# Optimization experiments

Hardware: AMD Instinct MI355X
Metric: run time of the kernel (lower is better)

The kernel has to match this reference:

```python
import jax, jax.numpy as jnp
import numpy as np

N_NODES = 50000
N_EDGES = 1600000
IN_DIM = 128
HID = [128, 128]
OUT_DIM = 64
N_USERS = 10000


def setup_inputs() -> dict:
    key = jax.random.key(0)
    ks = jax.random.split(key, 12)
    features = jax.random.normal(ks[0], (N_NODES, IN_DIM), jnp.float32)
    src = jax.random.randint(ks[1], (N_EDGES,), 0, N_NODES)
    dst = jax.random.randint(ks[2], (N_EDGES,), 0, N_NODES)
    users = jax.random.randint(ks[3], (N_USERS,), 0, N_NODES)
    s = 0.05
    W0 = jax.random.normal(ks[4], (IN_DIM, HID[0]), jnp.float32) * s
    b0 = jnp.zeros((HID[0],), jnp.float32)
    W1 = jax.random.normal(ks[5], (HID[0], HID[1]), jnp.float32) * s
    b1 = jnp.zeros((HID[1],), jnp.float32)
    Ws1 = jax.random.normal(ks[6], (HID[1], 64), jnp.float32) * s
    bs1 = jnp.zeros((64,), jnp.float32)
    Ws2 = jax.random.normal(ks[7], (64, OUT_DIM), jnp.float32) * s
    bs2 = jnp.zeros((OUT_DIM,), jnp.float32)
    return {"features": features, "W0": W0, "b0": b0, "W1": W1, "b1": b1,
            "Ws1": Ws1, "bs1": bs1, "Ws2": Ws2, "bs2": bs2,
            "src": src, "dst": dst, "users": users}


def _gcn_layer(h, src, dst, cs, cd, W, b):
    # DGL GraphConv, norm='both': relu(D_in^-1/2 A D_out^-1/2 (h W) + b)
    h = h @ W                                   # [N, d_out]
    m = (h * cs)[src]                           # [E, d_out] gathered messages
    agg = jax.ops.segment_sum(m, dst, num_segments=N_NODES)
    return jax.nn.relu(agg * cd + b)


def reference(features, W0, b0, W1, b1, Ws1, bs1, Ws2, bs2, src, dst, users):
    ones = jnp.ones(src.shape[0], jnp.float32)
    deg_out = jax.ops.segment_sum(ones, src, num_segments=N_NODES)
    deg_in = jax.ops.segment_sum(ones, dst, num_segments=N_NODES)
    cs = jnp.maximum(deg_out, 1.0)[:, None] ** -0.5  # source-side norm
    cd = jnp.maximum(deg_in, 1.0)[:, None] ** -0.5   # dest-side norm
    h = _gcn_layer(features, src, dst, cs, cd, W0, b0)
    # dropout between layers: identity in eval mode
    h = _gcn_layer(h, src, dst, cs, cd, W1, b1)
    user_h = h[users]                            # [U, HID[-1]]
    R = jnp.tanh(user_h @ Ws1 + bs1) @ Ws2 + bs2  # SR head
    return (R, h)
```

## Files before the change

kernel.cpp:

```cpp
#include <hip/hip_runtime.h>
#include <hip/hip_bf16.h>
#include <hip/hip_fp16.h>

#define NN 50000
#define NE 1600000
#define DIM 128
#define NU 10000
#define NB 256
#define SLICE_W 12500
#define NE4 (NE / 4)
#define CHUNK4 ((NE4 + NB - 1) / NB)
#define NSC 49

__global__ __launch_bounds__(512) void k_hist(const int4* __restrict__ src4,
                                              const int4* __restrict__ dst4,
                                              unsigned int* __restrict__ histD,
                                              unsigned int* __restrict__ histS) {
    __shared__ unsigned int lh[SLICE_W];
    for (int i = threadIdx.x; i < SLICE_W; i += 512) lh[i] = 0u;
    __syncthreads();
    int b = blockIdx.x & (NB - 1);
    const int4* idx4 = (blockIdx.x < NB) ? dst4 : src4;
    unsigned int* out = ((blockIdx.x < NB) ? histD : histS) + (size_t)b * SLICE_W;
    int beg = b * CHUNK4, end = min(beg + CHUNK4, NE4);
    for (int i = beg + threadIdx.x; i < end; i += 512) {
        int4 v = idx4[i];
        atomicAdd(&lh[v.x >> 2], 1u << ((v.x & 3) * 8));
        atomicAdd(&lh[v.y >> 2], 1u << ((v.y & 3) * 8));
        atomicAdd(&lh[v.z >> 2], 1u << ((v.z & 3) * 8));
        atomicAdd(&lh[v.w >> 2], 1u << ((v.w & 3) * 8));
    }
    __syncthreads();
    for (int i = threadIdx.x; i < SLICE_W; i += 512) out[i] = lh[i];
}

__global__ __launch_bounds__(256) void k_reduce_norms(const unsigned int* __restrict__ histD,
                                                      const unsigned int* __restrict__ histS,
                                                      int* __restrict__ din,
                                                      float* __restrict__ cs, float* __restrict__ cd,
                                                      int* __restrict__ partials) {
    __shared__ int red[256];
    int wi = blockIdx.x * blockDim.x + threadIdx.x;
    unsigned int d0 = 0, d1 = 0, d2 = 0, d3 = 0, s0 = 0, s1 = 0, s2 = 0, s3 = 0;
    if (wi < SLICE_W) {
        for (int b = 0; b < NB; ++b) {
            unsigned int wd = histD[(size_t)b * SLICE_W + wi];
            unsigned int ws = histS[(size_t)b * SLICE_W + wi];
            d0 += wd & 0xFFu; d1 += (wd >> 8) & 0xFFu; d2 += (wd >> 16) & 0xFFu; d3 += wd >> 24;
            s0 += ws & 0xFFu; s1 += (ws >> 8) & 0xFFu; s2 += (ws >> 16) & 0xFFu; s3 += ws >> 24;
        }
        int n = wi * 4;
        *(int4*)&din[n] = make_int4(d0, d1, d2, d3);
        float4 vcd, vcs;
        vcd.x = rsqrtf(fmaxf((float)d0, 1.f)); vcd.y = rsqrtf(fmaxf((float)d1, 1.f));
        vcd.z = rsqrtf(fmaxf((float)d2, 1.f)); vcd.w = rsqrtf(fmaxf((float)d3, 1.f));
        vcs.x = rsqrtf(fmaxf((float)s0, 1.f)); vcs.y = rsqrtf(fmaxf((float)s1, 1.f));
        vcs.z = rsqrtf(fmaxf((float)s2, 1.f)); vcs.w = rsqrtf(fmaxf((float)s3, 1.f));
        *(float4*)&cd[n] = vcd;
        *(float4*)&cs[n] = vcs;
    }
    red[threadIdx.x] = (int)(d0 + d1 + d2 + d3);
    __syncthreads();
    for (int off = 128; off > 0; off >>= 1) {
        if (threadIdx.x < off) red[threadIdx.x] += red[threadIdx.x + off];
        __syncthreads();
    }
    if (threadIdx.x == 0) partials[blockIdx.x] = red[0];
}

__global__ __launch_bounds__(64) void k_scan2(const int* __restrict__ partials,
                                              int* __restrict__ bases) {
    int lane = threadIdx.x;
    int v = (lane < NSC) ? partials[lane] : 0;
    int s = v;
    for (int off = 1; off < 64; off <<= 1) {
        int n = __shfl_up(s, off);
        if (lane >= off) s += n;
    }
    if (lane < NSC) bases[lane] = s - v;
}

__global__ __launch_bounds__(256) void k_scan3(const int* __restrict__ din,
                                               const int* __restrict__ bases,
                                               int* __restrict__ offs) {
    __shared__ int part[256];
    int t = threadIdx.x;
    int n0 = blockIdx.x * 1024 + t * 4;
    int4 d = make_int4(0, 0, 0, 0);
    if (n0 < NN) d = *(const int4*)&din[n0];
    int tsum = d.x + d.y + d.z + d.w;
    part[t] = tsum;
    __syncthreads();
    for (int off = 1; off < 256; off <<= 1) {
        int v = (t >= off) ? part[t - off] : 0;
        __syncthreads();
        part[t] += v;
        __syncthreads();
    }
    if (n0 < NN) {
        int o = bases[blockIdx.x] + part[t] - tsum;
        *(int4*)&offs[n0] = make_int4(o, o + d.x, o + d.x + d.y, o + d.x + d.y + d.z);
    }
}

__global__ __launch_bounds__(256) void k_blockbase(const unsigned int* __restrict__ histD,
                                                   unsigned char* __restrict__ rel8) {
    int n = blockIdx.x * blockDim.x + threadIdx.x;
    if (n >= NN) return;
    int wi = n >> 2, sh = (n & 3) * 8;
    unsigned int run = 0;
    for (int b = 0; b < NB; ++b) {
        rel8[(size_t)b * NN + n] = (unsigned char)run;
        run += (histD[(size_t)b * SLICE_W + wi] >> sh) & 0xFFu;
    }
}

__global__ __launch_bounds__(512) void k_scatter2(const int4* __restrict__ src4,
                                                  const int4* __restrict__ dst4,
                                                  const int* __restrict__ offs,
                                                  const unsigned char* __restrict__ rel8,
                                                  int* __restrict__ csc) {
    __shared__ unsigned int lc[SLICE_W];
    for (int i = threadIdx.x; i < SLICE_W; i += 512) lc[i] = 0u;
    __syncthreads();
    int b = blockIdx.x;
    const unsigned char* rel = rel8 + (size_t)b * NN;
    int beg = b * CHUNK4, end = min(beg + CHUNK4, NE4);
    for (int i = beg + threadIdx.x; i < end; i += 512) {
        int4 s = src4[i];
        int4 d = dst4[i];
#pragma unroll
        for (int j = 0; j < 4; ++j) {
            int dd = (j == 0) ? d.x : (j == 1) ? d.y : (j == 2) ? d.z : d.w;
            int ss = (j == 0) ? s.x : (j == 1) ? s.y : (j == 2) ? s.z : s.w;
            int sh = (dd & 3) * 8;
            unsigned int old = atomicAdd(&lc[dd >> 2], 1u << sh);
            int local = (old >> sh) & 0xFF;
            csc[offs[dd] + rel[dd] + local] = ss;
        }
    }
}

__global__ __launch_bounds__(256) void k_matmul_cs(const float* __restrict__ X,
                                                   const float* __restrict__ W,
                                                   const float* __restrict__ cs,
                                                   __half* __restrict__ Y, int nrows) {
    __shared__ __half sW[DIM * DIM];
    __shared__ float sX[16][DIM];
    for (int i = threadIdx.x * 4; i < DIM * DIM; i += 256 * 4) {
        float4 w4 = *(const float4*)&W[i];
        *(__half2*)&sW[i]     = __float22half2_rn(make_float2(w4.x, w4.y));
        *(__half2*)&sW[i + 2] = __float22half2_rn(make_float2(w4.z, w4.w));
    }
    int rl = threadIdx.x >> 6;
    int c = (threadIdx.x & 63) * 2;
    int ngroups = (nrows + 15) >> 4;
    for (int g = blockIdx.x; g < ngroups; g += gridDim.x) {
        __syncthreads();
        {
            int row = threadIdx.x >> 4;
            int col = (threadIdx.x & 15) * 8;
            int rr = min(g * 16 + row, nrows - 1);
            const float* xp = X + (size_t)rr * DIM + col;
            *(float4*)&sX[row][col] = *(const float4*)xp;
            *(float4*)&sX[row][col + 4] = *(const float4*)(xp + 4);
        }
        __syncthreads();
        float acc[4][2] = {};
#pragma unroll 4
        for (int k = 0; k < DIM; ++k) {
            float2 w = __half22float2(*(const __half2*)&sW[k * DIM + c]);
            float x0 = sX[rl * 4 + 0][k];
            float x1 = sX[rl * 4 + 1][k];
            float x2 = sX[rl * 4 + 2][k];
            float x3 = sX[rl * 4 + 3][k];
            acc[0][0] = fmaf(x0, w.x, acc[0][0]); acc[0][1] = fmaf(x0, w.y, acc[0][1]);
            acc[1][0] = fmaf(x1, w.x, acc[1][0]); acc[1][1] = fmaf(x1, w.y, acc[1][1]);
            acc[2][0] = fmaf(x2, w.x, acc[2][0]); acc[2][1] = fmaf(x2, w.y, acc[2][1]);
            acc[3][0] = fmaf(x3, w.x, acc[3][0]); acc[3][1] = fmaf(x3, w.y, acc[3][1]);
        }
#pragma unroll
        for (int j = 0; j < 4; ++j) {
            int r = g * 16 + rl * 4 + j;
            if (r < nrows) {
                float s = cs[r];
                __half2 hv = __float22half2_rn(make_float2(acc[j][0] * s, acc[j][1] * s));
                *(__half2*)&Y[(size_t)r * DIM + c] = hv;
            }
        }
    }
}

__global__ __launch_bounds__(256) void k_aggregate(const __half* __restrict__ hs,
                                                   const int* __restrict__ csc,
                                                   const int* __restrict__ offs,
                                                   const int* __restrict__ din,
                                                   const float* __restrict__ cd,
                                                   const float* __restrict__ bias,
                                                   float* __restrict__ out) {
    int wid = threadIdx.x >> 6;
    int lane = threadIdx.x & 63;
    int h = lane >> 5;
    int l = lane & 31;
    int d = blockIdx.x * 4 + wid;
    int beg = offs[d];
    int end = beg + din[d];
    const __half* base = hs + l * 4;
    float a0 = 0.f, a1 = 0.f, a2 = 0.f, a3 = 0.f;
    float b0 = 0.f, b1 = 0.f, b2 = 0.f, b3 = 0.f;
    float c0 = 0.f, c1 = 0.f, c2 = 0.f, c3 = 0.f;
    float e0 = 0.f, e1 = 0.f, e2 = 0.f, e3 = 0.f;
    int i = beg + h;
    for (; i + 14 < end; i += 16) {
        int sI[8];
#pragma unroll
        for (int j = 0; j < 8; ++j) sI[j] = csc[i + 2 * j];
        short4 vI[8];
#pragma unroll
        for (int j = 0; j < 8; ++j) vI[j] = *(const short4*)(base + (size_t)sI[j] * DIM);
#pragma unroll
        for (int j = 0; j < 8; j += 4) {
            float2 x0 = __half22float2(*(const __half2*)&vI[j].x);
            float2 x1 = __half22float2(*(const __half2*)&vI[j].z);
            float2 y0 = __half22float2(*(const __half2*)&vI[j + 1].x);
            float2 y1 = __half22float2(*(const __half2*)&vI[j + 1].z);
            float2 z0 = __half22float2(*(const __half2*)&vI[j + 2].x);
            float2 z1 = __half22float2(*(const __half2*)&vI[j + 2].z);
            float2 w0 = __half22float2(*(const __half2*)&vI[j + 3].x);
            float2 w1 = __half22float2(*(const __half2*)&vI[j + 3].z);
            a0 += x0.x; a1 += x0.y; a2 += x1.x; a3 += x1.y;
            b0 += y0.x; b1 += y0.y; b2 += y1.x; b3 += y1.y;
            c0 += z0.x; c1 += z0.y; c2 += z1.x; c3 += z1.y;
            e0 += w0.x; e1 += w0.y; e2 += w1.x; e3 += w1.y;
        }
    }
    for (; i + 6 < end; i += 8) {
        int s0 = csc[i], s1 = csc[i + 2], s2 = csc[i + 4], s3 = csc[i + 6];
        short4 v0 = *(const short4*)(base + (size_t)s0 * DIM);
        short4 v1 = *(const short4*)(base + (size_t)s1 * DIM);
        short4 v2 = *(const short4*)(base + (size_t)s2 * DIM);
        short4 v3 = *(const short4*)(base + (size_t)s3 * DIM);
        float2 x0 = __half22float2(*(const __half2*)&v0.x);
        float2 x1 = __half22float2(*(const __half2*)&v0.z);
        float2 y0 = __half22float2(*(const __half2*)&v1.x);
        float2 y1 = __half22float2(*(const __half2*)&v1.z);
        float2 z0 = __half22float2(*(const __half2*)&v2.x);
        float2 z1 = __half22float2(*(const __half2*)&v2.z);
        float2 w0 = __half22float2(*(const __half2*)&v3.x);
        float2 w1 = __half22float2(*(const __half2*)&v3.z);
        a0 += x0.x; a1 += x0.y; a2 += x1.x; a3 += x1.y;
        b0 += y0.x; b1 += y0.y; b2 += y1.x; b3 += y1.y;
        c0 += z0.x; c1 += z0.y; c2 += z1.x; c3 += z1.y;
        e0 += w0.x; e1 += w0.y; e2 += w1.x; e3 += w1.y;
    }
    for (; i < end; i += 2) {
        int s = csc[i];
        short4 v = *(const short4*)(base + (size_t)s * DIM);
        float2 x0 = __half22float2(*(const __half2*)&v.x);
        float2 x1 = __half22float2(*(const __half2*)&v.z);
        a0 += x0.x; a1 += x0.y; a2 += x1.x; a3 += x1.y;
    }
    a0 += b0 + c0 + e0; a1 += b1 + c1 + e1;
    a2 += b2 + c2 + e2; a3 += b3 + c3 + e3;
    a0 += __shfl(a0, lane ^ 32);
    a1 += __shfl(a1, lane ^ 32);
    a2 += __shfl(a2, lane ^ 32);
    a3 += __shfl(a3, lane ^ 32);
    if (h == 0) {
        float c = cd[d];
        float4 bv = *(const float4*)&bias[l * 4];
        float4 o;
        o.x = fmaxf(fmaf(a0, c, bv.x), 0.f);
        o.y = fmaxf(fmaf(a1, c, bv.y), 0.f);
        o.z = fmaxf(fmaf(a2, c, bv.z), 0.f);
        o.w = fmaxf(fmaf(a3, c, bv.w), 0.f);
        *(float4*)&out[(size_t)d * DIM + l * 4] = o;
    }
}

__global__ __launch_bounds__(256) void k_sr_head(const float* __restrict__ h,
                                                 const int* __restrict__ users,
                                                 const float* __restrict__ Ws1,
                                                 const float* __restrict__ bs1,
                                                 const float* __restrict__ Ws2,
                                                 const float* __restrict__ bs2,
                                                 float* __restrict__ R, int nu) {
    __shared__ float sW1[DIM * 64];
    __shared__ float sW2[64 * 64];
    __shared__ float sU[4][DIM];
    __shared__ float sT[4][64];
    for (int i = threadIdx.x * 4; i < DIM * 64; i += 256 * 4)
        *(float4*)&sW1[i] = *(const float4*)&Ws1[i];
    for (int i = threadIdx.x * 4; i < 64 * 64; i += 256 * 4)
        *(float4*)&sW2[i] = *(const float4*)&Ws2[i];
    int ul = threadIdx.x >> 6;
    int c = threadIdx.x & 63;
    for (int base = blockIdx.x * 4; base < nu; base += gridDim.x * 4) {
        int u = base + ul;
        __syncthreads();
        if (u < nu) {
            int node = users[u];
            *(float2*)&sU[ul][c * 2] = *(const float2*)&h[(size_t)node * DIM + c * 2];
        }
        __syncthreads();
        float t = 0.f;
        if (u < nu) {
            float acc = bs1[c];
#pragma unroll 8
            for (int k = 0; k < DIM; ++k) acc = fmaf(sU[ul][k], sW1[k * 64 + c], acc);
            t = tanhf(acc);
        }
        sT[ul][c] = t;
        __syncthreads();
        if (u < nu) {
            float acc = bs2[c];
#pragma unroll 8
            for (int k = 0; k < 64; ++k) acc = fmaf(sT[ul][k], sW2[k * 64 + c], acc);
            R[(size_t)u * 64 + c] = acc;
        }
    }
}

extern "C" void kernel_launch(void* const* d_in, const int* in_sizes, int n_in,
                              void* d_out, int out_size, void* d_ws, size_t ws_size,
                              hipStream_t stream) {
    const float* features = (const float*)d_in[0];
    const float* W0  = (const float*)d_in[1];
    const float* b0  = (const float*)d_in[2];
    const float* W1  = (const float*)d_in[3];
    const float* b1  = (const float*)d_in[4];
    const float* Ws1 = (const float*)d_in[5];
    const float* bs1 = (const float*)d_in[6];
    const float* Ws2 = (const float*)d_in[7];
    const float* bs2 = (const float*)d_in[8];
    const int* src   = (const int*)d_in[9];
    const int* dst   = (const int*)d_in[10];
    const int* users = (const int*)d_in[11];

    float* R = (float*)d_out;
    float* H = (float*)d_out + (size_t)NU * 64;

    char* ws = (char*)d_ws;
    __half* hsA  = (__half*)(ws + 0);
    unsigned int* histD = (unsigned int*)(ws + 0);
    unsigned int* histS = (unsigned int*)(ws + 12800000);
    unsigned char* rel8 = (unsigned char*)(ws + 12800000);
    int* csc     = (int*)(ws + 25600000);
    int*   din   = (int*)  (ws + 32000000);
    float* cs    = (float*)(ws + 32200000);
    float* cd    = (float*)(ws + 32400000);
    int*   offs  = (int*)  (ws + 32600000);
    int*   partials = (int*)(ws + 32800000);
    int*   bases    = (int*)(ws + 32801024);

    k_hist<<<2 * NB, 512, 0, stream>>>((const int4*)src, (const int4*)dst, histD, histS);
    k_reduce_norms<<<NSC, 256, 0, stream>>>(histD, histS, din, cs, cd, partials);
    k_scan2<<<1, 64, 0, stream>>>(partials, bases);
    k_scan3<<<NSC, 256, 0, stream>>>(din, bases, offs);
    k_blockbase<<<(NN + 255) / 256, 256, 0, stream>>>(histD, rel8);
    k_scatter2<<<NB, 512, 0, stream>>>((const int4*)src, (const int4*)dst, offs, rel8, csc);

    k_matmul_cs<<<1024, 256, 0, stream>>>(features, W0, cs, hsA, NN);
    k_aggregate<<<12500, 256, 0, stream>>>(hsA, csc, offs, din, cd, b0, H);

    k_matmul_cs<<<1024, 256, 0, stream>>>(H, W1, cs, hsA, NN);
    k_aggregate<<<12500, 256, 0, stream>>>(hsA, csc, offs, din, cd, b1, H);

    k_sr_head<<<625, 256, 0, stream>>>(H, users, Ws1, bs1, Ws2, bs2, R, NU);
}
```

Before: 294.6 us.

## Split aggregation feature columns into XCD-aligned chunks for L2 locality

The aggregation kernel now splits the 128-wide feature row into four 32-column chunks. Each chunk is handled by blocks that map to a pair of XCDs through the blockIdx-mod-8 round-robin, so each XCD's L2 only caches a quarter of the gathered fp16 feature table. Each wave now processes 8 edges in parallel with 8 lanes per edge and 8-byte loads, and reduces across slots with three shuffle rounds. The grid grows fourfold and each destination's CSC indices are read four times. The per-lane loads are only 64 bytes per row segment, so row gathers become less coalesced.

```diff
diff --git a/kernel.cpp b/kernel.cpp
--- a/kernel.cpp
+++ b/kernel.cpp
@@ -198,44 +198,25 @@
                                                    const float* __restrict__ cd,
                                                    const float* __restrict__ bias,
                                                    float* __restrict__ out) {
+    int bid = blockIdx.x;
+    int xcd = bid & 7;
+    int chunk = xcd >> 1;
+    int g = (bid >> 3) * 2 + (bid & 1);
     int wid = threadIdx.x >> 6;
     int lane = threadIdx.x & 63;
-    int h = lane >> 5;
-    int l = lane & 31;
-    int d = blockIdx.x * 4 + wid;
+    int slot = lane >> 3;
+    int l = lane & 7;
+    int d = g * 4 + wid;
     int beg = offs[d];
     int end = beg + din[d];
-    const __half* base = hs + l * 4;
+    const __half* base = hs + chunk * 32 + l * 4;
     float a0 = 0.f, a1 = 0.f, a2 = 0.f, a3 = 0.f;
     float b0 = 0.f, b1 = 0.f, b2 = 0.f, b3 = 0.f;
     float c0 = 0.f, c1 = 0.f, c2 = 0.f, c3 = 0.f;
     float e0 = 0.f, e1 = 0.f, e2 = 0.f, e3 = 0.f;
-    int i = beg + h;
-    for (; i + 14 < end; i += 16) {
-        int sI[8];
-#pragma unroll
-        for (int j = 0; j < 8; ++j) sI[j] = csc[i + 2 * j];
-        short4 vI[8];
-#pragma unroll
-        for (int j = 0; j < 8; ++j) vI[j] = *(const short4*)(base + (size_t)sI[j] * DIM);
-#pragma unroll
-        for (int j = 0; j < 8; j += 4) {
-            float2 x0 = __half22float2(*(const __half2*)&vI[j].x);
-            float2 x1 = __half22float2(*(const __half2*)&vI[j].z);
-            float2 y0 = __half22float2(*(const __half2*)&vI[j + 1].x);
-            float2 y1 = __half22float2(*(const __half2*)&vI[j + 1].z);
-            float2 z0 = __half22float2(*(const __half2*)&vI[j + 2].x);
-            float2 z1 = __half22float2(*(const __half2*)&vI[j + 2].z);
-            float2 w0 = __half22float2(*(const __half2*)&vI[j + 3].x);
-            float2 w1 = __half22float2(*(const __half2*)&vI[j + 3].z);
-            a0 += x0.x; a1 += x0.y; a2 += x1.x; a3 += x1.y;
-            b0 += y0.x; b1 += y0.y; b2 += y1.x; b3 += y1.y;
-            c0 += z0.x; c1 += z0.y; c2 += z1.x; c3 += z1.y;
-            e0 += w0.x; e1 += w0.y; e2 += w1.x; e3 += w1.y;
-        }
-    }
-    for (; i + 6 < end; i += 8) {
-        int s0 = csc[i], s1 = csc[i + 2], s2 = csc[i + 4], s3 = csc[i + 6];
+    int i = beg + slot;
+    for (; i + 24 < end; i += 32) {
+        int s0 = csc[i], s1 = csc[i + 8], s2 = csc[i + 16], s3 = csc[i + 24];
         short4 v0 = *(const short4*)(base + (size_t)s0 * DIM);
         short4 v1 = *(const short4*)(base + (size_t)s1 * DIM);
         short4 v2 = *(const short4*)(base + (size_t)s2 * DIM);
@@ -253,7 +234,7 @@
         c0 += z0.x; c1 += z0.y; c2 += z1.x; c3 += z1.y;
         e0 += w0.x; e1 += w0.y; e2 += w1.x; e3 += w1.y;
     }
-    for (; i < end; i += 2) {
+    for (; i < end; i += 8) {
         int s = csc[i];
         short4 v = *(const short4*)(base + (size_t)s * DIM);
         float2 x0 = __half22float2(*(const __half2*)&v.x);
@@ -262,19 +243,21 @@
     }
     a0 += b0 + c0 + e0; a1 += b1 + c1 + e1;
     a2 += b2 + c2 + e2; a3 += b3 + c3 + e3;
-    a0 += __shfl(a0, lane ^ 32);
-    a1 += __shfl(a1, lane ^ 32);
-    a2 += __shfl(a2, lane ^ 32);
-    a3 += __shfl(a3, lane ^ 32);
-    if (h == 0) {
+    a0 += __shfl(a0, lane ^ 8);  a1 += __shfl(a1, lane ^ 8);
+    a2 += __shfl(a2, lane ^ 8);  a3 += __shfl(a3, lane ^ 8);
+    a0 += __shfl(a0, lane ^ 16); a1 += __shfl(a1, lane ^ 16);
+    a2 += __shfl(a2, lane ^ 16); a3 += __shfl(a3, lane ^ 16);
+    a0 += __shfl(a0, lane ^ 32); a1 += __shfl(a1, lane ^ 32);
+    a2 += __shfl(a2, lane ^ 32); a3 += __shfl(a3, lane ^ 32);
+    if (slot == 0) {
         float c = cd[d];
-        float4 bv = *(const float4*)&bias[l * 4];
+        float4 bv = *(const float4*)&bias[chunk * 32 + l * 4];
         float4 o;
         o.x = fmaxf(fmaf(a0, c, bv.x), 0.f);
         o.y = fmaxf(fmaf(a1, c, bv.y), 0.f);
         o.z = fmaxf(fmaf(a2, c, bv.z), 0.f);
         o.w = fmaxf(fmaf(a3, c, bv.w), 0.f);
-        *(float4*)&out[(size_t)d * DIM + l * 4] = o;
+        *(float4*)&out[(size_t)d * DIM + chunk * 32 + l * 4] = o;
     }
 }
 
@@ -361,10 +344,10 @@
     k_scatter2<<<NB, 512, 0, stream>>>((const int4*)src, (const int4*)dst, offs, rel8, csc);
 
     k_matmul_cs<<<1024, 256, 0, stream>>>(features, W0, cs, hsA, NN);
-    k_aggregate<<<12500, 256, 0, stream>>>(hsA, csc, offs, din, cd, b0, H);
+    k_aggregate<<<50000, 256, 0, stream>>>(hsA, csc, offs, din, cd, b0, H);
 
     k_matmul_cs<<<1024, 256, 0, stream>>>(H, W1, cs, hsA, NN);
-    k_aggregate<<<12500, 256, 0, stream>>>(hsA, csc, offs, din, cd, b1, H);
+    k_aggregate<<<50000, 256, 0, stream>>>(hsA, csc, offs, din, cd, b1, H);
 
     k_sr_head<<<625, 256, 0, stream>>>(H, users, Ws1, bs1, Ws2, bs2, R, NU);
 }
```

Result: slower. 393.7 us (+33.6%).
